# Performance work log

Hardware: AMD Instinct MI355X
Metric: run time of the kernel (lower is better)

The kernel has to match this reference:

```python
import jax, jax.numpy as jnp
import numpy as np

N_S, N_C, N_L = 100000, 20000, 5000
E_U, E_T = 2000000, 500000
D_S, D_C, D_L, H = 64, 32, 128, 128
N_LAYERS = 3  # num_layers=2 -> ModuleList holds 3 hetero layers


def _sage(h_src, h_dst, src_idx, dst_idx, W_self, W_neigh, b, n_dst):
    # DGL SAGEConv 'mean': fc_self(h_dst) + fc_neigh(mean of in-neighbor src feats) + bias
    summed = jax.ops.segment_sum(h_src[src_idx], dst_idx, num_segments=n_dst)  # [n_dst, d]
    deg = jax.ops.segment_sum(jnp.ones((src_idx.shape[0],), h_src.dtype), dst_idx, num_segments=n_dst)
    h_neigh = summed / jnp.maximum(deg, 1.0)[:, None]
    return h_dst @ W_self + h_neigh @ W_neigh + b


def setup_inputs() -> dict:
    key = jax.random.key(0)
    ks = jax.random.split(key, 24)
    s = 0.05
    inp = {
        'feat_student': jax.random.normal(ks[0], (N_S, D_S), jnp.float32),
        'feat_concept': jax.random.normal(ks[1], (N_C, D_C), jnp.float32),
        'feat_lecture': jax.random.normal(ks[2], (N_L, D_L), jnp.float32),
        'W_fs': jax.random.normal(ks[3], (D_S, H), jnp.float32) * s,
        'b_fs': jnp.zeros((H,), jnp.float32),
        'W_fc': jax.random.normal(ks[4], (D_C, H), jnp.float32) * s,
        'b_fc': jnp.zeros((H,), jnp.float32),
        'W_fl': jax.random.normal(ks[5], (D_L, H), jnp.float32) * s,
        'b_fl': jnp.zeros((H,), jnp.float32),
        # per-layer, per-relation SAGE params (all dims 128 so they stack)
        'W_self_u': jax.random.normal(ks[6], (N_LAYERS, H, H), jnp.float32) * s,
        'W_neigh_u': jax.random.normal(ks[7], (N_LAYERS, H, H), jnp.float32) * s,
        'b_u': jnp.zeros((N_LAYERS, H), jnp.float32),
        'W_self_t': jax.random.normal(ks[8], (N_LAYERS, H, H), jnp.float32) * s,
        'W_neigh_t': jax.random.normal(ks[9], (N_LAYERS, H, H), jnp.float32) * s,
        'b_t': jnp.zeros((N_LAYERS, H), jnp.float32),
        'und_src': jax.random.randint(ks[10], (E_U,), 0, N_S, jnp.int32),
        'und_dst': jax.random.randint(ks[11], (E_U,), 0, N_C, jnp.int32),
        'tea_src': jax.random.randint(ks[12], (E_T,), 0, N_L, jnp.int32),
        'tea_dst': jax.random.randint(ks[13], (E_T,), 0, N_C, jnp.int32),
    }
    return inp


def reference(feat_student, feat_concept, feat_lecture,
              W_fs, b_fs, W_fc, b_fc, W_fl, b_fl,
              W_self_u, W_neigh_u, b_u, W_self_t, W_neigh_t, b_t,
              und_src, und_dst, tea_src, tea_dst):
    # input projections per node type
    h_s = feat_student @ W_fs + b_fs
    h_c = feat_concept @ W_fc + b_fc
    h_l = feat_lecture @ W_fl + b_fl
    n_c = h_c.shape[0]
    for i in range(N_LAYERS):
        ou = _sage(h_s, h_c, und_src, und_dst, W_self_u[i], W_neigh_u[i], b_u[i], n_c)
        ot = _sage(h_l, h_c, tea_src, tea_dst, W_self_t[i], W_neigh_t[i], b_t[i], n_c)
        # HeteroGraphConv cross-relation aggregate: 'mean' on layer 0, default 'sum' after
        h_c = (ou + ot) * (0.5 if i == 0 else 1.0)
        if i != N_LAYERS - 1:
            h_c = jax.nn.relu(h_c)  # dropout is identity in eval mode
        # student/lecture are never destination types -> features pass through
    return h_c  # [N_C, 128] concept embeddings
```

## Files before the change

### kernel.cpp

```cpp
#include <hip/hip_runtime.h>
#include <hip/hip_bf16.h>
#include <cstdint>
#include <cstddef>

#define NS_ 100000
#define NC_ 20000
#define NL_ 5000
#define EU_ 2000000
#define ET_ 500000
#define H_  128

#define NBK_ 625
#define CHK_ 3907
#define UBLK_ 512
#define TBLK_ 128
#define CAPU_ 3600
#define CAPT_ 1024
#define SEDGE_ 3712
#define SROW_ 640

typedef __attribute__((ext_vector_type(8))) short bs8;
typedef __attribute__((ext_vector_type(4))) float f32x4;
typedef __attribute__((ext_vector_type(2))) float v2f;

__device__ inline short bf_rne(float f) {
    unsigned u = __float_as_uint(f);
    u = (u + 0x7fffu + ((u >> 16) & 1u)) >> 16;
    return (short)u;
}
__device__ inline unsigned pack_bf16x2(float a, float b) {
    return ((unsigned)(unsigned short)bf_rne(a)) |
           (((unsigned)(unsigned short)bf_rne(b)) << 16);
}
__device__ inline float bflo(unsigned w) { return __uint_as_float(w << 16); }
__device__ inline float bfhi(unsigned w) { return __uint_as_float(w & 0xffff0000u); }

#define B_SCU UBLK_
#define B_SCT TBLK_
#define B_CVT 512
#define B_PACK 480
#define B_BC 2
#define B_WFC 16
#define B_TOTAL (B_SCU + B_SCT + B_CVT + B_PACK + B_BC + B_WFC)

__global__ __launch_bounds__(256) void prep_fused_kernel(
    const int* __restrict__ und_dst, const int* __restrict__ tea_dst,
    unsigned* __restrict__ CUm, unsigned* __restrict__ CTm,
    const float* __restrict__ feat_s, unsigned* __restrict__ fs8,
    const float* __restrict__ feat_l, unsigned* __restrict__ flb,
    const float* __restrict__ Wsu, const float* __restrict__ Wnu,
    const float* __restrict__ Wst, const float* __restrict__ Wnt,
    const float* __restrict__ W_fs, const float* __restrict__ W_fl,
    short* __restrict__ WpL,
    const float* __restrict__ bu, const float* __restrict__ bt,
    const float* __restrict__ b_fs, const float* __restrict__ b_fl,
    float* __restrict__ bc,
    const float* __restrict__ W_fc, short* __restrict__ WpC)
{
    __shared__ unsigned cnt[768];
    const int b = blockIdx.x;
    const int tid = threadIdx.x;

    if (b < B_SCU + B_SCT) {
        const bool isU = (b < B_SCU);
        const int blk = isU ? b : (b - B_SCU);
        const int nEdge = isU ? EU_ : ET_;
        const int* dstp = isU ? und_dst : tea_dst;
        unsigned* Cm = isU ? CUm : CTm;
        for (int i = tid; i < 768; i += 256) cnt[i] = 0;
        __syncthreads();
        const int start = blk * CHK_;
        const int end = min(start + CHK_, nEdge);
        for (int i = start + tid; i < end; i += 256)
            atomicAdd(&cnt[dstp[i] >> 5], 1u);
        __syncthreads();
        for (int i = tid; i < NBK_; i += 256)
            Cm[(size_t)blk * SROW_ + i] = cnt[i];
    } else if (b < B_SCU + B_SCT + B_CVT) {
        int i = (b - B_SCU - B_SCT) * 256 + tid;
        const int stride = B_CVT * 256;
        const int nS = NS_ * 16;
        const int nTot = nS + NL_ * 64;
        for (; i < nTot; i += stride) {
            if (i < nS) {
                const float4 v = ((const float4*)feat_s)[i];
                unsigned r = __builtin_amdgcn_cvt_pk_fp8_f32(v.x, v.y, 0, false);
                r = __builtin_amdgcn_cvt_pk_fp8_f32(v.z, v.w, r, true);
                fs8[i] = r;
            } else {
                int j = i - nS;
                float2 v = ((const float2*)feat_l)[j];
                flb[j] = pack_bf16x2(v.x, v.y);
            }
        }
    } else if (b < B_SCU + B_SCT + B_CVT + B_PACK) {
        int i = (b - B_SCU - B_SCT - B_CVT) * 256 + tid;
        int j = i & 7;
        int lane = (i >> 3) & 63;
        int nt = (i >> 9) & 7;
        int ktAll = i >> 12;
        int l = ktAll / 10;
        int kt = ktAll - l * 10;
        int k = kt * 32 + (lane >> 4) * 8 + j;
        int n = nt * 16 + (lane & 15);
        const size_t WL = (size_t)l * H_ * H_;
        float v;
        if (k < 128) {
            v = Wsu[WL + k * H_ + n] + Wst[WL + k * H_ + n];
        } else if (k < 192) {
            int a = k - 128;
            v = 0.f;
            for (int t = 0; t < 128; t++) v += W_fs[a * H_ + t] * Wnu[WL + t * H_ + n];
        } else {
            int a = k - 192;
            v = 0.f;
            for (int t = 0; t < 128; t++) v += W_fl[a * H_ + t] * Wnt[WL + t * H_ + n];
        }
        WpL[i] = bf_rne(v);
    } else if (b < B_SCU + B_SCT + B_CVT + B_PACK + B_BC) {
        int i = (b - B_SCU - B_SCT - B_CVT - B_PACK) * 256 + tid;
        if (i < 3 * H_) {
            int l = i >> 7, c = i & 127;
            const size_t WL = (size_t)l * H_ * H_;
            float v = bu[i] + bt[i];
            for (int j2 = 0; j2 < 128; j2++)
                v += b_fs[j2] * Wnu[WL + j2 * H_ + c] + b_fl[j2] * Wnt[WL + j2 * H_ + c];
            bc[i] = v;
        }
    } else {
        int i = (b - (B_SCU + B_SCT + B_CVT + B_PACK + B_BC)) * 256 + tid;
        int j = i & 7;
        int lane = (i >> 3) & 63;
        int nt = (i >> 9) & 7;
        int k = (lane >> 4) * 8 + j;
        int n = nt * 16 + (lane & 15);
        WpC[i] = bf_rne(W_fc[k * H_ + n]);
    }
}

__global__ __launch_bounds__(256) void scan_kernel(
    const unsigned* __restrict__ CUm, const unsigned* __restrict__ CTm,
    unsigned* __restrict__ OUm, unsigned* __restrict__ OTm,
    unsigned* __restrict__ gcurU, unsigned* __restrict__ gcurT)
{
    __shared__ unsigned part[4][64];
    const int b = blockIdx.x;
    const int tid = threadIdx.x;
    const int s = tid >> 6;
    const int kl = tid & 63;
    const int k = b * 64 + kl;
    const bool ok = (k < NBK_);

    {
        unsigned run = 0;
        const int r0 = s * 128;
        if (ok) {
#pragma unroll 8
            for (int r = r0; r < r0 + 128; ++r)
                run += CUm[(size_t)r * SROW_ + k];
        }
        part[s][kl] = run;
        __syncthreads();
        unsigned base = 0;
        for (int s2 = 0; s2 < s; ++s2) base += part[s2][kl];
        if (ok && s == 3) gcurU[k] = base + run;
        if (ok) {
            unsigned acc = base;
#pragma unroll 8
            for (int r = r0; r < r0 + 128; ++r) {
                unsigned c = CUm[(size_t)r * SROW_ + k];
                OUm[(size_t)r * SROW_ + k] = acc;
                acc += c;
            }
        }
        __syncthreads();
    }
    {
        unsigned run = 0;
        const int r0 = s * 32;
        if (ok) {
#pragma unroll 8
            for (int r = r0; r < r0 + 32; ++r)
                run += CTm[(size_t)r * SROW_ + k];
        }
        part[s][kl] = run;
        __syncthreads();
        unsigned base = 0;
        for (int s2 = 0; s2 < s; ++s2) base += part[s2][kl];
        if (ok && s == 3) gcurT[k] = base + run;
        if (ok) {
            unsigned acc = base;
#pragma unroll 8
            for (int r = r0; r < r0 + 32; ++r) {
                unsigned c = CTm[(size_t)r * SROW_ + k];
                OTm[(size_t)r * SROW_ + k] = acc;
                acc += c;
            }
        }
    }
}

__global__ __launch_bounds__(256) void scatter_kernel(
    const int* __restrict__ und_dst, const int* __restrict__ und_src,
    const int* __restrict__ tea_dst, const int* __restrict__ tea_src,
    const unsigned* __restrict__ CUm, const unsigned* __restrict__ CTm,
    const unsigned* __restrict__ OUm, const unsigned* __restrict__ OTm,
    unsigned* __restrict__ binnedU, unsigned* __restrict__ binnedT)
{
    __shared__ unsigned smem[5760];
    const int b = blockIdx.x;
    const int tid = threadIdx.x;
    const bool isU = (b < B_SCU);
    const int blk = isU ? b : (b - B_SCU);
    const int nEdge = isU ? EU_ : ET_;
    const int* dstp = isU ? und_dst : tea_dst;
    const int* srcp = isU ? und_src : tea_src;
    const unsigned* Cm = isU ? CUm : CTm;
    const unsigned* Om = isU ? OUm : OTm;
    unsigned* binned = isU ? binnedU : binnedT;
    const unsigned cap = isU ? CAPU_ : CAPT_;
    unsigned* sed = smem;
    unsigned* cnt = smem + 3968;
    unsigned* pre = smem + 4736;
    unsigned* par = smem + 5504;

    unsigned Wr[3];
#pragma unroll
    for (int r = 0; r < 3; r++) {
        int k = r * 256 + tid;
        cnt[k] = (k < NBK_) ? Cm[(size_t)blk * SROW_ + k] : 0;
        Wr[r] = (k < NBK_) ? Om[(size_t)blk * SROW_ + k] : 0;
    }
    __syncthreads();
    unsigned c0 = cnt[3 * tid], c1 = cnt[3 * tid + 1], c2 = cnt[3 * tid + 2];
    unsigned s = c0 + c1 + c2;
    par[tid] = s;
    __syncthreads();
    unsigned sum = s;
    for (int d = 1; d < 256; d <<= 1) {
        unsigned x = (tid >= d) ? par[tid - d] : 0;
        __syncthreads();
        sum += x;
        par[tid] = sum;
        __syncthreads();
    }
    unsigned p = sum - s;
    pre[3 * tid] = p;
    pre[3 * tid + 1] = p + c0;
    pre[3 * tid + 2] = p + c0 + c1;
    __syncthreads();
#pragma unroll
    for (int r = 0; r < 3; r++) {
        int k = r * 256 + tid;
        if (k < NBK_) {
            unsigned L = cnt[k];
            unsigned W = Wr[r];
            if (W + L > cap) W = (L <= cap) ? cap - L : 0;
            cnt[k] = k * cap + W - pre[k];
        }
    }
    __syncthreads();
    const int start = blk * CHK_;
    const int end = min(start + CHK_, nEdge);
    for (int i = start + tid; i < end; i += 256) {
        int d = dstp[i];
        unsigned k = (unsigned)d >> 5;
        unsigned e = (unsigned)srcp[i] | ((unsigned)(d & 31) << 17) | (k << 22);
        unsigned pos = atomicAdd(&pre[k], 1u);
        sed[pos] = e;
    }
    __syncthreads();
    const int n = end - start;
    for (int i = tid; i < n; i += 256) {
        unsigned e = sed[i];
        binned[cnt[e >> 22] + i] = e & 0x3FFFFFu;
    }
}

__global__ __launch_bounds__(256) void agg_kernel(
    const unsigned* __restrict__ gcurU, const unsigned* __restrict__ binnedU,
    const uint2* __restrict__ fs8, unsigned* __restrict__ aggFu,
    const unsigned* __restrict__ gcurT, const unsigned* __restrict__ binnedT,
    const uint4* __restrict__ flb4, unsigned* __restrict__ aggFt)
{
    __shared__ unsigned sedge[SEDGE_];
    __shared__ unsigned sh[32], soff[33], scur[32];
    const int b = blockIdx.x;
    const int tid = threadIdx.x;
    const bool isU = (b < NBK_);
    const int bb = isU ? b : (b - NBK_);
    const unsigned* binned = isU ? binnedU : binnedT;
    const unsigned cap = isU ? CAPU_ : CAPT_;
    const size_t start = (size_t)bb * cap;
    const int n = min((int)(isU ? gcurU : gcurT)[bb], (int)cap);

    if (tid < 32) sh[tid] = 0;
    __syncthreads();
    for (int i = tid; i < n; i += 256)
        atomicAdd(&sh[(binned[start + i] >> 17) & 31], 1u);
    __syncthreads();
    if (tid == 0) {
        unsigned r = 0;
        for (int j = 0; j < 32; j++) {
            unsigned v = sh[j];
            soff[j] = r;
            scur[j] = r;
            r += v;
        }
        soff[32] = r;
    }
    __syncthreads();
    for (int i = tid; i < n; i += 256) {
        unsigned p = binned[start + i];
        unsigned pos = atomicAdd(&scur[(p >> 17) & 31], 1u);
        if (pos < SEDGE_) sedge[pos] = p & 0x1FFFFu;
    }
    __syncthreads();

    const int g = tid >> 3;
    const int sub = tid & 7;
    const int gs = (int)soff[g];
    const int ge = (int)min(soff[g + 1], (unsigned)SEDGE_);
    const int c = bb * 32 + g;
    const float inv = 1.f / (float)max(ge - gs, 1);

    if (isU) {
        float a[8];
#pragma unroll
        for (int i = 0; i < 8; i++) a[i] = 0.f;
        int e = gs;
        for (; e + 2 <= ge; e += 2) {
            unsigned s0 = sedge[e], s1 = sedge[e + 1];
            uint2 w0 = fs8[(size_t)s0 * 8 + sub];
            uint2 w1 = fs8[(size_t)s1 * 8 + sub];
            v2f p0 = __builtin_amdgcn_cvt_pk_f32_fp8(w0.x, false);
            v2f p1 = __builtin_amdgcn_cvt_pk_f32_fp8(w0.x, true);
            v2f p2 = __builtin_amdgcn_cvt_pk_f32_fp8(w0.y, false);
            v2f p3 = __builtin_amdgcn_cvt_pk_f32_fp8(w0.y, true);
            a[0] += p0.x; a[1] += p0.y; a[2] += p1.x; a[3] += p1.y;
            a[4] += p2.x; a[5] += p2.y; a[6] += p3.x; a[7] += p3.y;
            p0 = __builtin_amdgcn_cvt_pk_f32_fp8(w1.x, false);
            p1 = __builtin_amdgcn_cvt_pk_f32_fp8(w1.x, true);
            p2 = __builtin_amdgcn_cvt_pk_f32_fp8(w1.y, false);
            p3 = __builtin_amdgcn_cvt_pk_f32_fp8(w1.y, true);
            a[0] += p0.x; a[1] += p0.y; a[2] += p1.x; a[3] += p1.y;
            a[4] += p2.x; a[5] += p2.y; a[6] += p3.x; a[7] += p3.y;
        }
        if (e < ge) {
            uint2 w0 = fs8[(size_t)sedge[e] * 8 + sub];
            v2f p0 = __builtin_amdgcn_cvt_pk_f32_fp8(w0.x, false);
            v2f p1 = __builtin_amdgcn_cvt_pk_f32_fp8(w0.x, true);
            v2f p2 = __builtin_amdgcn_cvt_pk_f32_fp8(w0.y, false);
            v2f p3 = __builtin_amdgcn_cvt_pk_f32_fp8(w0.y, true);
            a[0] += p0.x; a[1] += p0.y; a[2] += p1.x; a[3] += p1.y;
            a[4] += p2.x; a[5] += p2.y; a[6] += p3.x; a[7] += p3.y;
        }
        uint4 o;
        o.x = pack_bf16x2(a[0] * inv, a[1] * inv);
        o.y = pack_bf16x2(a[2] * inv, a[3] * inv);
        o.z = pack_bf16x2(a[4] * inv, a[5] * inv);
        o.w = pack_bf16x2(a[6] * inv, a[7] * inv);
        ((uint4*)aggFu)[(size_t)c * 8 + sub] = o;
    } else {
        float a[16];
#pragma unroll
        for (int i = 0; i < 16; i++) a[i] = 0.f;
        for (int e = gs; e < ge; e++) {
            unsigned src = sedge[e];
            uint4 w0 = flb4[(size_t)src * 16 + sub * 2];
            uint4 w1 = flb4[(size_t)src * 16 + sub * 2 + 1];
            a[0] += bflo(w0.x); a[1] += bfhi(w0.x);
            a[2] += bflo(w0.y); a[3] += bfhi(w0.y);
            a[4] += bflo(w0.z); a[5] += bfhi(w0.z);
            a[6] += bflo(w0.w); a[7] += bfhi(w0.w);
            a[8]  += bflo(w1.x); a[9]  += bfhi(w1.x);
            a[10] += bflo(w1.y); a[11] += bfhi(w1.y);
            a[12] += bflo(w1.z); a[13] += bfhi(w1.z);
            a[14] += bflo(w1.w); a[15] += bfhi(w1.w);
        }
        uint4 o0, o1;
        o0.x = pack_bf16x2(a[0] * inv, a[1] * inv);
        o0.y = pack_bf16x2(a[2] * inv, a[3] * inv);
        o0.z = pack_bf16x2(a[4] * inv, a[5] * inv);
        o0.w = pack_bf16x2(a[6] * inv, a[7] * inv);
        o1.x = pack_bf16x2(a[8] * inv, a[9] * inv);
        o1.y = pack_bf16x2(a[10] * inv, a[11] * inv);
        o1.z = pack_bf16x2(a[12] * inv, a[13] * inv);
        o1.w = pack_bf16x2(a[14] * inv, a[15] * inv);
        ((uint4*)aggFt)[(size_t)c * 16 + sub * 2] = o0;
        ((uint4*)aggFt)[(size_t)c * 16 + sub * 2 + 1] = o1;
    }
}

__global__ __launch_bounds__(256) void layers_fused_kernel(
    const float* __restrict__ feat_c, const short* __restrict__ WpC,
    const float* __restrict__ b_fc,
    const unsigned* __restrict__ aggFu, const unsigned* __restrict__ aggFt,
    const short* __restrict__ WpL, const float* __restrict__ bc,
    float* __restrict__ out)
{
    __shared__ short lds[4][16 * 132];
    const int tid = threadIdx.x;
    const int lane = tid & 63;
    const int wv = tid >> 6;
    const int row0 = blockIdx.x * 64 + wv * 16;
    const int q = lane >> 4;
    const int m = lane & 15;
    const int rA = min(row0 + m, NC_ - 1);
    short* tile = lds[wv];

    bs8 fuF[2], ftF[4], hcF[4];
#pragma unroll
    for (int kt = 0; kt < 2; kt++)
        fuF[kt] = *(const bs8*)(aggFu + (size_t)rA * 32 + kt * 16 + q * 4);
#pragma unroll
    for (int kt = 0; kt < 4; kt++)
        ftF[kt] = *(const bs8*)(aggFt + (size_t)rA * 64 + kt * 16 + q * 4);

    f32x4 acc[8];
#pragma unroll
    for (int i = 0; i < 8; i++) acc[i] = (f32x4){0.f, 0.f, 0.f, 0.f};
    {
        const float* xp = feat_c + (size_t)rA * 32 + q * 8;
        float4 xa = *(const float4*)xp;
        float4 xb = *(const float4*)(xp + 4);
        bs8 af;
        af[0] = bf_rne(xa.x); af[1] = bf_rne(xa.y); af[2] = bf_rne(xa.z); af[3] = bf_rne(xa.w);
        af[4] = bf_rne(xb.x); af[5] = bf_rne(xb.y); af[6] = bf_rne(xb.z); af[7] = bf_rne(xb.w);
#pragma unroll
        for (int nt = 0; nt < 8; nt++) {
            bs8 bfr = *(const bs8*)(WpC + ((size_t)nt * 64 + lane) * 8);
            acc[nt] = __builtin_amdgcn_mfma_f32_16x16x32_bf16(af, bfr, acc[nt], 0, 0, 0);
        }
    }
#pragma unroll
    for (int nt = 0; nt < 8; nt++) {
        int col = nt * 16 + m;
        float bv = b_fc[col];
#pragma unroll
        for (int r = 0; r < 4; r++)
            tile[(q * 4 + r) * 132 + col] = bf_rne(acc[nt][r] + bv);
    }
#pragma unroll
    for (int kt = 0; kt < 4; kt++)
        hcF[kt] = *(const bs8*)(tile + m * 132 + kt * 32 + q * 8);

#pragma unroll
    for (int l = 0; l < 3; l++) {
#pragma unroll
        for (int i = 0; i < 8; i++) acc[i] = (f32x4){0.f, 0.f, 0.f, 0.f};
        const short* wl = WpL + (size_t)l * 40960;
#pragma unroll
        for (int kt = 0; kt < 10; kt++) {
            bs8 af = (kt < 4) ? hcF[kt] : ((kt < 6) ? fuF[kt - 4] : ftF[kt - 6]);
            const short* wp = wl + (size_t)kt * 4096;
#pragma unroll
            for (int nt = 0; nt < 8; nt++) {
                bs8 bfr = *(const bs8*)(wp + ((size_t)nt * 64 + lane) * 8);
                acc[nt] = __builtin_amdgcn_mfma_f32_16x16x32_bf16(af, bfr, acc[nt], 0, 0, 0);
            }
        }
        const float scale = (l == 0) ? 0.5f : 1.0f;
        const float* bl = bc + l * H_;
        if (l < 2) {
#pragma unroll
            for (int nt = 0; nt < 8; nt++) {
                int col = nt * 16 + m;
                float bv = bl[col];
#pragma unroll
                for (int r = 0; r < 4; r++)
                    tile[(q * 4 + r) * 132 + col] =
                        bf_rne(fmaxf((acc[nt][r] + bv) * scale, 0.f));
            }
#pragma unroll
            for (int kt = 0; kt < 4; kt++)
                hcF[kt] = *(const bs8*)(tile + m * 132 + kt * 32 + q * 8);
        } else {
#pragma unroll
            for (int nt = 0; nt < 8; nt++) {
                int col = nt * 16 + m;
                float bv = bl[col];
#pragma unroll
                for (int r = 0; r < 4; r++) {
                    int row = row0 + q * 4 + r;
                    if (row < NC_)
                        out[(size_t)row * H_ + col] = (acc[nt][r] + bv) * scale;
                }
            }
        }
    }
}

extern "C" void kernel_launch(void* const* d_in, const int* in_sizes, int n_in,
                              void* d_out, int out_size, void* d_ws, size_t ws_size,
                              hipStream_t stream)
{
    (void)in_sizes; (void)n_in; (void)out_size; (void)ws_size;
    const float* feat_s = (const float*)d_in[0];
    const float* feat_c = (const float*)d_in[1];
    const float* feat_l = (const float*)d_in[2];
    const float* W_fs = (const float*)d_in[3];
    const float* b_fs = (const float*)d_in[4];
    const float* W_fc = (const float*)d_in[5];
    const float* b_fc = (const float*)d_in[6];
    const float* W_fl = (const float*)d_in[7];
    const float* b_fl = (const float*)d_in[8];
    const float* W_self_u  = (const float*)d_in[9];
    const float* W_neigh_u = (const float*)d_in[10];
    const float* b_u = (const float*)d_in[11];
    const float* W_self_t  = (const float*)d_in[12];
    const float* W_neigh_t = (const float*)d_in[13];
    const float* b_t = (const float*)d_in[14];
    const int* und_src = (const int*)d_in[15];
    const int* und_dst = (const int*)d_in[16];
    const int* tea_src = (const int*)d_in[17];
    const int* tea_dst = (const int*)d_in[18];
    float* out = (float*)d_out;

    char* ws = (char*)d_ws;
    size_t o = 0;
    auto alloc = [&](size_t bytes) -> char* {
        char* p = ws + o;
        o += (bytes + 255) & ~(size_t)255;
        return p;
    };
    unsigned* fs8  = (unsigned*)alloc((size_t)NS_ * 16 * 4);
    unsigned* flb  = (unsigned*)alloc((size_t)NL_ * 64 * 4);
    unsigned* aggFu = (unsigned*)alloc((size_t)NC_ * 32 * 4);
    unsigned* aggFt = (unsigned*)alloc((size_t)NC_ * 64 * 4);
    short* WpL = (short*)alloc((size_t)3 * 10 * 8 * 64 * 8 * 2);
    short* WpC = (short*)alloc((size_t)8 * 64 * 8 * 2);
    float* bc  = (float*)alloc((size_t)3 * H_ * 4);
    unsigned* gcurU = (unsigned*)alloc((size_t)NBK_ * 4);
    unsigned* gcurT = (unsigned*)alloc((size_t)NBK_ * 4);
    unsigned* binnedU = (unsigned*)alloc((size_t)NBK_ * CAPU_ * 4);
    unsigned* binnedT = (unsigned*)alloc((size_t)NBK_ * CAPT_ * 4);

    unsigned* CUm = aggFt;
    unsigned* OUm = aggFt + (size_t)UBLK_ * SROW_;
    unsigned* CTm = aggFt + (size_t)2 * UBLK_ * SROW_;
    unsigned* OTm = CTm + (size_t)TBLK_ * SROW_;

    prep_fused_kernel<<<B_TOTAL, 256, 0, stream>>>(
        und_dst, tea_dst, CUm, CTm,
        feat_s, fs8, feat_l, flb,
        W_self_u, W_neigh_u, W_self_t, W_neigh_t, W_fs, W_fl, WpL,
        b_u, b_t, b_fs, b_fl, bc,
        W_fc, WpC);

    scan_kernel<<<10, 256, 0, stream>>>(CUm, CTm, OUm, OTm, gcurU, gcurT);

    scatter_kernel<<<B_SCU + B_SCT, 256, 0, stream>>>(
        und_dst, und_src, tea_dst, tea_src,
        CUm, CTm, OUm, OTm, binnedU, binnedT);

    agg_kernel<<<2 * NBK_, 256, 0, stream>>>(
        gcurU, binnedU, (const uint2*)fs8, aggFu,
        gcurT, binnedT, (const uint4*)flb, aggFt);

    layers_fused_kernel<<<(NC_ + 63) / 64, 256, 0, stream>>>(
        feat_c, WpC, b_fc, aggFu, aggFt, WpL, bc, out);
}
```

Baseline: 222.5 us.

## Unroll gather loops deeper and split layer GEMM columns across wave pairs

New measurement: 207.1 us. 1.07x faster.

```diff
diff --git a/kernel.cpp b/kernel.cpp
--- a/kernel.cpp
+++ b/kernel.cpp
@@ -329,14 +329,18 @@
 #pragma unroll
         for (int i = 0; i < 8; i++) a[i] = 0.f;
         int e = gs;
-        for (; e + 2 <= ge; e += 2) {
+        for (; e + 4 <= ge; e += 4) {
             unsigned s0 = sedge[e], s1 = sedge[e + 1];
+            unsigned s2 = sedge[e + 2], s3 = sedge[e + 3];
             uint2 w0 = fs8[(size_t)s0 * 8 + sub];
             uint2 w1 = fs8[(size_t)s1 * 8 + sub];
-            v2f p0 = __builtin_amdgcn_cvt_pk_f32_fp8(w0.x, false);
-            v2f p1 = __builtin_amdgcn_cvt_pk_f32_fp8(w0.x, true);
-            v2f p2 = __builtin_amdgcn_cvt_pk_f32_fp8(w0.y, false);
-            v2f p3 = __builtin_amdgcn_cvt_pk_f32_fp8(w0.y, true);
+            uint2 w2 = fs8[(size_t)s2 * 8 + sub];
+            uint2 w3 = fs8[(size_t)s3 * 8 + sub];
+            v2f p0, p1, p2, p3;
+            p0 = __builtin_amdgcn_cvt_pk_f32_fp8(w0.x, false);
+            p1 = __builtin_amdgcn_cvt_pk_f32_fp8(w0.x, true);
+            p2 = __builtin_amdgcn_cvt_pk_f32_fp8(w0.y, false);
+            p3 = __builtin_amdgcn_cvt_pk_f32_fp8(w0.y, true);
             a[0] += p0.x; a[1] += p0.y; a[2] += p1.x; a[3] += p1.y;
             a[4] += p2.x; a[5] += p2.y; a[6] += p3.x; a[7] += p3.y;
             p0 = __builtin_amdgcn_cvt_pk_f32_fp8(w1.x, false);
@@ -345,8 +349,20 @@
             p3 = __builtin_amdgcn_cvt_pk_f32_fp8(w1.y, true);
             a[0] += p0.x; a[1] += p0.y; a[2] += p1.x; a[3] += p1.y;
             a[4] += p2.x; a[5] += p2.y; a[6] += p3.x; a[7] += p3.y;
-        }
-        if (e < ge) {
+            p0 = __builtin_amdgcn_cvt_pk_f32_fp8(w2.x, false);
+            p1 = __builtin_amdgcn_cvt_pk_f32_fp8(w2.x, true);
+            p2 = __builtin_amdgcn_cvt_pk_f32_fp8(w2.y, false);
+            p3 = __builtin_amdgcn_cvt_pk_f32_fp8(w2.y, true);
+            a[0] += p0.x; a[1] += p0.y; a[2] += p1.x; a[3] += p1.y;
+            a[4] += p2.x; a[5] += p2.y; a[6] += p3.x; a[7] += p3.y;
+            p0 = __builtin_amdgcn_cvt_pk_f32_fp8(w3.x, false);
+            p1 = __builtin_amdgcn_cvt_pk_f32_fp8(w3.x, true);
+            p2 = __builtin_amdgcn_cvt_pk_f32_fp8(w3.y, false);
+            p3 = __builtin_amdgcn_cvt_pk_f32_fp8(w3.y, true);
+            a[0] += p0.x; a[1] += p0.y; a[2] += p1.x; a[3] += p1.y;
+            a[4] += p2.x; a[5] += p2.y; a[6] += p3.x; a[7] += p3.y;
+        }
+        for (; e < ge; e++) {
             uint2 w0 = fs8[(size_t)sedge[e] * 8 + sub];
             v2f p0 = __builtin_amdgcn_cvt_pk_f32_fp8(w0.x, false);
             v2f p1 = __builtin_amdgcn_cvt_pk_f32_fp8(w0.x, true);
@@ -365,7 +381,31 @@
         float a[16];
 #pragma unroll
         for (int i = 0; i < 16; i++) a[i] = 0.f;
-        for (int e = gs; e < ge; e++) {
+        int e = gs;
+        for (; e + 2 <= ge; e += 2) {
+            unsigned s0 = sedge[e], s1 = sedge[e + 1];
+            uint4 w0 = flb4[(size_t)s0 * 16 + sub * 2];
+            uint4 w1 = flb4[(size_t)s0 * 16 + sub * 2 + 1];
+            uint4 x0 = flb4[(size_t)s1 * 16 + sub * 2];
+            uint4 x1 = flb4[(size_t)s1 * 16 + sub * 2 + 1];
+            a[0] += bflo(w0.x); a[1] += bfhi(w0.x);
+            a[2] += bflo(w0.y); a[3] += bfhi(w0.y);
+            a[4] += bflo(w0.z); a[5] += bfhi(w0.z);
+            a[6] += bflo(w0.w); a[7] += bfhi(w0.w);
+            a[8]  += bflo(w1.x); a[9]  += bfhi(w1.x);
+            a[10] += bflo(w1.y); a[11] += bfhi(w1.y);
+            a[12] += bflo(w1.z); a[13] += bfhi(w1.z);
+            a[14] += bflo(w1.w); a[15] += bfhi(w1.w);
+            a[0] += bflo(x0.x); a[1] += bfhi(x0.x);
+            a[2] += bflo(x0.y); a[3] += bfhi(x0.y);
+            a[4] += bflo(x0.z); a[5] += bfhi(x0.z);
+            a[6] += bflo(x0.w); a[7] += bfhi(x0.w);
+            a[8]  += bflo(x1.x); a[9]  += bfhi(x1.x);
+            a[10] += bflo(x1.y); a[11] += bfhi(x1.y);
+            a[12] += bflo(x1.z); a[13] += bfhi(x1.z);
+            a[14] += bflo(x1.w); a[15] += bfhi(x1.w);
+        }
+        if (e < ge) {
             unsigned src = sedge[e];
             uint4 w0 = flb4[(size_t)src * 16 + sub * 2];
             uint4 w1 = flb4[(size_t)src * 16 + sub * 2 + 1];
@@ -399,15 +439,17 @@
     const short* __restrict__ WpL, const float* __restrict__ bc,
     float* __restrict__ out)
 {
-    __shared__ short lds[4][16 * 132];
+    __shared__ short lds[2][16 * 132];
     const int tid = threadIdx.x;
     const int lane = tid & 63;
     const int wv = tid >> 6;
-    const int row0 = blockIdx.x * 64 + wv * 16;
+    const int gr = wv >> 1;
+    const int h = wv & 1;
+    const int row0 = blockIdx.x * 32 + gr * 16;
     const int q = lane >> 4;
     const int m = lane & 15;
     const int rA = min(row0 + m, NC_ - 1);
-    short* tile = lds[wv];
+    short* tile = lds[gr];
 
     bs8 fuF[2], ftF[4], hcF[4];
 #pragma unroll
@@ -417,9 +459,9 @@
     for (int kt = 0; kt < 4; kt++)
         ftF[kt] = *(const bs8*)(aggFt + (size_t)rA * 64 + kt * 16 + q * 4);
 
-    f32x4 acc[8];
-#pragma unroll
-    for (int i = 0; i < 8; i++) acc[i] = (f32x4){0.f, 0.f, 0.f, 0.f};
+    f32x4 acc[4];
+#pragma unroll
+    for (int i = 0; i < 4; i++) acc[i] = (f32x4){0.f, 0.f, 0.f, 0.f};
     {
         const float* xp = feat_c + (size_t)rA * 32 + q * 8;
         float4 xa = *(const float4*)xp;
@@ -428,35 +470,39 @@
         af[0] = bf_rne(xa.x); af[1] = bf_rne(xa.y); af[2] = bf_rne(xa.z); af[3] = bf_rne(xa.w);
         af[4] = bf_rne(xb.x); af[5] = bf_rne(xb.y); af[6] = bf_rne(xb.z); af[7] = bf_rne(xb.w);
 #pragma unroll
-        for (int nt = 0; nt < 8; nt++) {
-            bs8 bfr = *(const bs8*)(WpC + ((size_t)nt * 64 + lane) * 8);
+        for (int nt = 0; nt < 4; nt++) {
+            int ntg = h * 4 + nt;
+            bs8 bfr = *(const bs8*)(WpC + ((size_t)ntg * 64 + lane) * 8);
             acc[nt] = __builtin_amdgcn_mfma_f32_16x16x32_bf16(af, bfr, acc[nt], 0, 0, 0);
         }
     }
 #pragma unroll
-    for (int nt = 0; nt < 8; nt++) {
-        int col = nt * 16 + m;
+    for (int nt = 0; nt < 4; nt++) {
+        int col = (h * 4 + nt) * 16 + m;
         float bv = b_fc[col];
 #pragma unroll
         for (int r = 0; r < 4; r++)
             tile[(q * 4 + r) * 132 + col] = bf_rne(acc[nt][r] + bv);
     }
+    __syncthreads();
 #pragma unroll
     for (int kt = 0; kt < 4; kt++)
         hcF[kt] = *(const bs8*)(tile + m * 132 + kt * 32 + q * 8);
+    __syncthreads();
 
 #pragma unroll
     for (int l = 0; l < 3; l++) {
 #pragma unroll
-        for (int i = 0; i < 8; i++) acc[i] = (f32x4){0.f, 0.f, 0.f, 0.f};
+        for (int i = 0; i < 4; i++) acc[i] = (f32x4){0.f, 0.f, 0.f, 0.f};
         const short* wl = WpL + (size_t)l * 40960;
 #pragma unroll
         for (int kt = 0; kt < 10; kt++) {
             bs8 af = (kt < 4) ? hcF[kt] : ((kt < 6) ? fuF[kt - 4] : ftF[kt - 6]);
             const short* wp = wl + (size_t)kt * 4096;
 #pragma unroll
-            for (int nt = 0; nt < 8; nt++) {
-                bs8 bfr = *(const bs8*)(wp + ((size_t)nt * 64 + lane) * 8);
+            for (int nt = 0; nt < 4; nt++) {
+                int ntg = h * 4 + nt;
+                bs8 bfr = *(const bs8*)(wp + ((size_t)ntg * 64 + lane) * 8);
                 acc[nt] = __builtin_amdgcn_mfma_f32_16x16x32_bf16(af, bfr, acc[nt], 0, 0, 0);
             }
         }
@@ -464,21 +510,23 @@
         const float* bl = bc + l * H_;
         if (l < 2) {
 #pragma unroll
-            for (int nt = 0; nt < 8; nt++) {
-                int col = nt * 16 + m;
+            for (int nt = 0; nt < 4; nt++) {
+                int col = (h * 4 + nt) * 16 + m;
                 float bv = bl[col];
 #pragma unroll
                 for (int r = 0; r < 4; r++)
                     tile[(q * 4 + r) * 132 + col] =
                         bf_rne(fmaxf((acc[nt][r] + bv) * scale, 0.f));
             }
+            __syncthreads();
 #pragma unroll
             for (int kt = 0; kt < 4; kt++)
                 hcF[kt] = *(const bs8*)(tile + m * 132 + kt * 32 + q * 8);
+            __syncthreads();
         } else {
 #pragma unroll
-            for (int nt = 0; nt < 8; nt++) {
-                int col = nt * 16 + m;
+            for (int nt = 0; nt < 4; nt++) {
+                int col = (h * 4 + nt) * 16 + m;
                 float bv = bl[col];
 #pragma unroll
                 for (int r = 0; r < 4; r++) {
@@ -558,6 +606,6 @@
         gcurU, binnedU, (const uint2*)fs8, aggFu,
         gcurT, binnedT, (const uint4*)flb, aggFt);
 
-    layers_fused_kernel<<<(NC_ + 63) / 64, 256, 0, stream>>>(
+    layers_fused_kernel<<<(NC_ + 31) / 32, 256, 0, stream>>>(
         feat_c, WpC, b_fc, aggFu, aggFt, WpL, bc, out);
 }
```
